# Kernel tuning notes

Measured on AMD Instinct MI355X. Metric: run time of the kernel, lower is better.

## Reference

```python
import jax, jax.numpy as jnp
import numpy as np
import math

B, T, E = 2, 2048, 1024
H = 16
D = E // H  # head_dim = 64

def setup_inputs() -> dict:
    key = jax.random.key(0)
    k1, k2, k3, k4, k5 = jax.random.split(key, 5)
    s = 0.02
    return {
        "x": jax.random.normal(k1, (B, T, E), dtype=jnp.float32),
        "W_attn": jax.random.normal(k2, (E, 3 * E), dtype=jnp.float32) * s,
        "b_attn": jax.random.normal(k3, (3 * E,), dtype=jnp.float32) * s,
        "W_proj": jax.random.normal(k4, (E, E), dtype=jnp.float32) * s,
        "b_proj": jax.random.normal(k5, (E,), dtype=jnp.float32) * s,
    }

def reference(x, W_attn, b_attn, W_proj, b_proj):
    Bx, Tx, Ex = x.shape
    qkv = x @ W_attn + b_attn                      # [B,T,3E]
    q, k, v = jnp.split(qkv, 3, axis=2)
    # [B,T,E] -> [B,H,T,D]
    def heads(t):
        return t.reshape(Bx, Tx, H, D).transpose(0, 2, 1, 3)
    q, k, v = heads(q), heads(k), heads(v)
    scores = jnp.einsum('bhqd,bhkd->bhqk', q, k) / math.sqrt(D)
    causal = jnp.tril(jnp.ones((Tx, Tx), dtype=bool))
    scores = jnp.where(causal, scores, -jnp.inf)
    attn = jax.nn.softmax(scores, axis=-1)
    out = jnp.einsum('bhqk,bhkd->bhqd', attn, v)   # [B,H,T,D]
    out = out.transpose(0, 2, 1, 3).reshape(Bx, Tx, Ex)
    return out @ W_proj + b_proj
```

## Files before the change

kernel.cpp:

```cpp
#include <hip/hip_runtime.h>


typedef unsigned short u16;
typedef unsigned int u32;
typedef __bf16 bf8 __attribute__((ext_vector_type(8)));
typedef float f32x4 __attribute__((ext_vector_type(4)));
typedef float f32x16 __attribute__((ext_vector_type(16)));
typedef u32 u32x4v __attribute__((ext_vector_type(4)));

__device__ __forceinline__ u16 f2b(float f) {
    return __builtin_bit_cast(u16, (__bf16)f);
}

__device__ __forceinline__ u32 pk2(float lo, float hi) {
    return (u32)f2b(lo) | ((u32)f2b(hi) << 16);
}

__device__ __forceinline__ f32x4 mfma16(bf8 a, bf8 b, f32x4 c) {
    return __builtin_amdgcn_mfma_f32_16x16x32_bf16(a, b, c, 0, 0, 0);
}

__device__ __forceinline__ f32x16 mfma32(bf8 a, bf8 b, f32x16 c) {
    return __builtin_amdgcn_mfma_f32_32x32x16_bf16(a, b, c, 0, 0, 0);
}

__device__ __forceinline__ float fexp2(float x) {
    return __builtin_amdgcn_exp2f(x);
}

__device__ __forceinline__ void gload_lds16(const u16* g, u16* l) {
    __builtin_amdgcn_global_load_lds(
        (__attribute__((address_space(1))) void*)(g),
        (__attribute__((address_space(3))) void*)(l), 16, 0, 0);
}

__global__ __launch_bounds__(256) void k_prep(const float* __restrict__ x,
                                              const float* __restrict__ Wa,
                                              const float* __restrict__ Wp,
                                              u16* __restrict__ Xb,
                                              u16* __restrict__ WtA,
                                              u16* __restrict__ WtP) {
    __shared__ float tile[64][65];
    int id = blockIdx.x, t = threadIdx.x;
    if (id < 4096) {
        int i = id * 256 + t;
        float4 v = ((const float4*)x)[i];
        ushort4 o;
        o.x = f2b(v.x); o.y = f2b(v.y); o.z = f2b(v.z); o.w = f2b(v.w);
        ((ushort4*)Xb)[i] = o;
        return;
    }
    const float* in; u16* out; int N, j;
    if (id < 4864) { j = id - 4096; in = Wa; out = WtA; N = 3072; }
    else           { j = id - 4864; in = Wp; out = WtP; N = 1024; }
    int k0 = (j & 15) * 64, n0 = (j >> 4) * 64;
    int c = t & 63, r0 = t >> 6;
#pragma unroll
    for (int i = 0; i < 16; ++i) {
        int r = r0 + i * 4;
        tile[r][c] = in[(size_t)(k0 + r) * N + n0 + c];
    }
    __syncthreads();
#pragma unroll
    for (int i = 0; i < 16; ++i) {
        int r = r0 + i * 4;
        out[(size_t)(n0 + r) * 1024 + k0 + c] = f2b(tile[c][r]);
    }
}

#define GEMM_STAGE(GA0, GA1, GB0, GB1, K, B)                                   \
    do {                                                                       \
        gload_lds16(GA0 + (K), As[B] + tid * 8);                               \
        gload_lds16(GA1 + (K), As[B] + (256 + tid) * 8);                       \
        gload_lds16(GB0 + (K), Bs[B] + tid * 8);                               \
        gload_lds16(GB1 + (K), Bs[B] + (256 + tid) * 8);                       \
    } while (0)

#define GEMM_CORE(Aptr, Bptr)                                                  \
    int tid = threadIdx.x;                                                     \
    int w = tid >> 6, lane = tid & 63, l16 = lane & 15, quad = lane >> 4;      \
    int m0 = blockIdx.x * 128, n0 = blockIdx.y * 128;                          \
    int wr = (w >> 1) * 64, wc = (w & 1) * 64;                                 \
    __shared__ u16 As[2][128 * 32];                                            \
    __shared__ u16 Bs[2][128 * 32];                                            \
    f32x4 acc[4][4];                                                           \
    _Pragma("unroll") for (int mi = 0; mi < 4; ++mi)                           \
        _Pragma("unroll") for (int ni = 0; ni < 4; ++ni)                       \
            _Pragma("unroll") for (int r = 0; r < 4; ++r) acc[mi][ni][r] = 0.f;\
    int srow0 = tid >> 2, srow1 = 64 + srow0;                                  \
    int slc = ((tid & 3) ^ ((tid >> 3) & 3)) * 8;      \
    const u16* gA0 = Aptr + (size_t)(m0 + srow0) * 1024 + slc;                 \
    const u16* gA1 = Aptr + (size_t)(m0 + srow1) * 1024 + slc;                 \
    const u16* gB0 = Bptr + (size_t)(n0 + srow0) * 1024 + slc;                 \
    const u16* gB1 = Bptr + (size_t)(n0 + srow1) * 1024 + slc;                 \
    int cq = (quad ^ ((l16 >> 1) & 3)) * 8;               \
    GEMM_STAGE(gA0, gA1, gB0, gB1, 0, 0);                                      \
    for (int it = 0; it < 32; ++it) {                                          \
        int pb = it & 1;                                                       \
        __syncthreads();                           \
        bf8 af[4], bf[4];                                                      \
        _Pragma("unroll") for (int mi = 0; mi < 4; ++mi)                       \
            af[mi] = *(const bf8*)(As[pb] + (wr + mi * 16 + l16) * 32 + cq);   \
        _Pragma("unroll") for (int ni = 0; ni < 4; ++ni)                       \
            bf[ni] = *(const bf8*)(Bs[pb] + (wc + ni * 16 + l16) * 32 + cq);   \
        if (it < 31) GEMM_STAGE(gA0, gA1, gB0, gB1, (it + 1) * 32, pb ^ 1);    \
        _Pragma("unroll") for (int mi = 0; mi < 4; ++mi)                       \
            _Pragma("unroll") for (int ni = 0; ni < 4; ++ni)                   \
                acc[mi][ni] = mfma16(af[mi], bf[ni], acc[mi][ni]);             \
    }

__global__ __launch_bounds__(256, 3) void k_qkv(const u16* __restrict__ Xb,
                                                const u16* __restrict__ WtA,
                                                const float* __restrict__ ba,
                                                u16* __restrict__ Qb,
                                                u16* __restrict__ Kb,
                                                u16* __restrict__ Vtb) {
    GEMM_CORE(Xb, WtA)
    int sel = n0 >> 10;
    u16* dst = sel == 0 ? Qb : (sel == 1 ? Kb : Vtb);
    const float qs = 0.18033688011112042f;
#pragma unroll
    for (int ni = 0; ni < 4; ++ni) {
        int n = n0 + wc + ni * 16 + l16;
        float bias = ba[n];
        int h = (n & 1023) >> 6;
        int d = n & 63;
#pragma unroll
        for (int mi = 0; mi < 4; ++mi)
#pragma unroll
            for (int r = 0; r < 4; ++r) {
                int m = m0 + wr + mi * 16 + quad * 4 + r;
                int bb = m >> 11, tt = m & 2047;
                float v = acc[mi][ni][r] + bias;
                size_t hb = (size_t)(bb * 16 + h);
                if (sel == 2)
                    dst[hb * 131072 + (size_t)(tt >> 6) * 4096 + d * 64 + (tt & 63)] = f2b(v);
                else
                    dst[(hb * 2048 + tt) * 64 + d] =
                        f2b(sel == 0 ? v * qs : v);
            }
    }
}

__global__ __launch_bounds__(256, 3) void k_proj(const u16* __restrict__ AO,
                                                 const u16* __restrict__ WtP,
                                                 const float* __restrict__ bp,
                                                 float* __restrict__ out) {
    GEMM_CORE(AO, WtP)
#pragma unroll
    for (int ni = 0; ni < 4; ++ni) {
        int n = n0 + wc + ni * 16 + l16;
        float bias = bp[n];
#pragma unroll
        for (int mi = 0; mi < 4; ++mi)
#pragma unroll
            for (int r = 0; r < 4; ++r) {
                int m = m0 + wr + mi * 16 + quad * 4 + r;
                out[(size_t)m * 1024 + n] = acc[mi][ni][r] + bias;
            }
    }
}


#define STAGE(KT, B) do {                                                     \
    int ci0_ = tid, ci1_ = 256 + tid;                                         \
    const u16* kt_ = Kh + (size_t)(KT) * 4096;                                \
    gload_lds16(kt_ + (ci0_ >> 3) * 64 +                                      \
                (((ci0_ & 7) ^ ((ci0_ >> 5) & 7)) * 8), KV[B][0] + ci0_ * 8); \
    gload_lds16(kt_ + (ci1_ >> 3) * 64 +                                      \
                (((ci1_ & 7) ^ ((ci1_ >> 5) & 7)) * 8), KV[B][0] + ci1_ * 8); \
    const u16* vt_ = Vh + (size_t)(KT) * 4096;                                \
    gload_lds16(vt_ + (ci0_ >> 3) * 64 +                                      \
                (((ci0_ & 7) ^ ((ci0_ >> 3) & 7)) * 8), KV[B][1] + ci0_ * 8); \
    gload_lds16(vt_ + (ci1_ >> 3) * 64 +                                      \
                (((ci1_ & 7) ^ ((ci1_ >> 3) & 7)) * 8), KV[B][1] + ci1_ * 8); \
} while (0)

#define PVSTEP(SG, BFR) do {                                                  \
    bf8 va_ = *(const bf8*)(vb_ + l31 * 64 +                                  \
                            (((2 * (SG) + h) ^ vswz) * 8));                   \
    bf8 vc_ = *(const bf8*)(vb_ + (32 + l31) * 64 +                           \
                            (((2 * (SG) + h) ^ vswz) * 8));                   \
    bf8 pf_ = __builtin_bit_cast(bf8, BFR);                                   \
    oT0 = mfma32(va_, pf_, oT0);                                              \
    oT1 = mfma32(vc_, pf_, oT1);                                              \
} while (0)

#define BFRAGS(PK, PP, B0, B1) do {                                           \
    B0[0] = h ? PP[2] : PK[0]; B0[1] = h ? PP[3] : PK[1];                     \
    B0[2] = h ? PK[2] : PP[0]; B0[3] = h ? PK[3] : PP[1];                     \
    B1[0] = h ? PP[6] : PK[4]; B1[1] = h ? PP[7] : PK[5];                     \
    B1[2] = h ? PK[6] : PP[4]; B1[3] = h ? PK[7] : PP[5];                     \
} while (0)

__global__ __launch_bounds__(256, 2) void k_attn(const u16* __restrict__ Qb,
                                                 const u16* __restrict__ Kb,
                                                 const u16* __restrict__ Vtb,
                                                 u16* __restrict__ AO) {
    int id = blockIdx.x;
    int bh = (id & 7) * 4 + ((id >> 3) & 3);
    int t  = 15 - (id >> 5);
    int tid = threadIdx.x;
    int w = tid >> 6, lane = tid & 63, l31 = lane & 31, h = lane >> 5;

    const u16* Qh = Qb  + (size_t)bh * 131072;
    const u16* Kh = Kb  + (size_t)bh * 131072;
    const u16* Vh = Vtb + (size_t)bh * 131072;

    __shared__ u16 KV[2][2][4096];

    int tq = t + 16 * w;
    int qr = tq * 32;
    int ktmax = tq >> 1;
    int nkt = ((t + 48) >> 1) + 1;

    bf8 qf[4];
#pragma unroll
    for (int s = 0; s < 4; ++s)
        qf[s] = *(const bf8*)(Qh + (size_t)(qr + l31) * 64 + s * 16 + h * 8);

    float l_acc = 0.f;
    f32x16 oT0, oT1;
#pragma unroll
    for (int r = 0; r < 16; ++r) { oT0[r] = 0.f; oT1[r] = 0.f; }

    int kswz = (l31 >> 2) & 7;
    int vswz = l31 & 7;

    STAGE(0, 0);
    for (int kt = 0; kt < nkt; ++kt) {
        int pb = kt & 1;
        __syncthreads();
        if (kt + 1 < nkt) STAGE(kt + 1, pb ^ 1);

        if (kt <= ktmax) {
            const u16* kb_ = KV[pb][0];
            const u16* vb_ = KV[pb][1];
            bool diag = (kt == ktmax);
            bool doK1 = !(diag && ((tq & 1) == 0));

            f32x16 sT0, sT1;
#pragma unroll
            for (int r = 0; r < 16; ++r) { sT0[r] = 0.f; sT1[r] = 0.f; }
#pragma unroll
            for (int s = 0; s < 4; ++s) {
                bf8 kf = *(const bf8*)(kb_ + l31 * 64 +
                                       (((2 * s + h) ^ kswz) * 8));
                sT0 = mfma32(kf, qf[s], sT0);
            }
            if (doK1) {
#pragma unroll
                for (int s = 0; s < 4; ++s) {
                    bf8 kf = *(const bf8*)(kb_ + (32 + l31) * 64 +
                                           (((2 * s + h) ^ kswz) * 8));
                    sT1 = mfma32(kf, qf[s], sT1);
                }
            }

            int kb0 = kt * 64, qg = qr + l31;
            if (diag) {
#pragma unroll
                for (int r = 0; r < 16; ++r) {
                    int krow = kb0 + (r & 3) + 8 * (r >> 2) + 4 * h;
                    sT0[r] = fexp2(krow <= qg ? sT0[r] : -1e30f);
                    l_acc += sT0[r];
                }
                if (doK1) {
#pragma unroll
                    for (int r = 0; r < 16; ++r) {
                        int krow = kb0 + 32 + (r & 3) + 8 * (r >> 2) + 4 * h;
                        sT1[r] = fexp2(krow <= qg ? sT1[r] : -1e30f);
                        l_acc += sT1[r];
                    }
                }
            } else {
#pragma unroll
                for (int r = 0; r < 16; ++r) {
                    sT0[r] = fexp2(sT0[r]); l_acc += sT0[r];
                }
#pragma unroll
                for (int r = 0; r < 16; ++r) {
                    sT1[r] = fexp2(sT1[r]); l_acc += sT1[r];
                }
            }

            u32 pka[8], ppa[8];
#pragma unroll
            for (int j = 0; j < 8; ++j)
                pka[j] = pk2(sT0[2 * j], sT0[2 * j + 1]);
#pragma unroll
            for (int j = 0; j < 8; ++j)
                ppa[j] = __shfl_xor(pka[j], 32, 64);
            u32x4v bf0, bf1;
            BFRAGS(pka, ppa, bf0, bf1);
            PVSTEP(0, bf0);
            PVSTEP(1, bf1);
            if (doK1) {
                u32 pkb[8], ppb[8];
#pragma unroll
                for (int j = 0; j < 8; ++j)
                    pkb[j] = pk2(sT1[2 * j], sT1[2 * j + 1]);
#pragma unroll
                for (int j = 0; j < 8; ++j)
                    ppb[j] = __shfl_xor(pkb[j], 32, 64);
                u32x4v bg0, bg1;
                BFRAGS(pkb, ppb, bg0, bg1);
                PVSTEP(2, bg0);
                PVSTEP(3, bg1);
            }
        }
    }

    __syncthreads();
    float lsum = l_acc + __shfl_xor(l_acc, 32, 64);
    float linv = __builtin_amdgcn_rcpf(lsum);

    u32* Ot = (u32*)(&KV[0][0][0]) + w * 1152;
#pragma unroll
    for (int j = 0; j < 8; ++j) {
        int col = 4 * (j >> 1) + 2 * h + (j & 1);
        Ot[l31 * 36 + col]      = pk2(oT0[2 * j] * linv, oT0[2 * j + 1] * linv);
        Ot[l31 * 36 + 16 + col] = pk2(oT1[2 * j] * linv, oT1[2 * j + 1] * linv);
    }
    asm volatile("s_waitcnt lgkmcnt(0)" ::: "memory");
    __builtin_amdgcn_sched_barrier(0);

    int q2 = lane >> 1, half = lane & 1;
    int eb = bh >> 4, eh = bh & 15;
    size_t row = (size_t)eb * 2048 + qr + q2;
    const u32* src = Ot + q2 * 36 + half * 16;
    u32* dstg = (u32*)(AO + row * 1024 + eh * 64) + half * 16;
#pragma unroll
    for (int c = 0; c < 4; ++c)
        *(u32x4v*)(dstg + 4 * c) = *(const u32x4v*)(src + 4 * c);
}

extern "C" void kernel_launch(void* const* d_in, const int* in_sizes, int n_in,
                              void* d_out, int out_size, void* d_ws, size_t ws_size,
                              hipStream_t stream) {
    const float* x  = (const float*)d_in[0];
    const float* Wa = (const float*)d_in[1];
    const float* ba = (const float*)d_in[2];
    const float* Wp = (const float*)d_in[3];
    const float* bp = (const float*)d_in[4];
    float* out = (float*)d_out;

    char* ws = (char*)d_ws;
    const size_t MB = 1024 * 1024;
    u16* Xb  = (u16*)(ws);
    u16* WtA = (u16*)(ws + 8  * MB);
    u16* WtP = (u16*)(ws + 14 * MB);
    u16* Qb  = (u16*)(ws + 16 * MB);
    u16* Kb  = (u16*)(ws + 24 * MB);
    u16* Vtb = (u16*)(ws + 32 * MB);
    u16* AO  = Xb;

    k_prep<<<dim3(5120),    dim3(256), 0, stream>>>(x, Wa, Wp, Xb, WtA, WtP);
    k_qkv <<<dim3(32, 24),  dim3(256), 0, stream>>>(Xb, WtA, ba, Qb, Kb, Vtb);
    k_attn<<<dim3(512),     dim3(256), 0, stream>>>(Qb, Kb, Vtb, AO);
    k_proj<<<dim3(32, 8),   dim3(256), 0, stream>>>(AO, WtP, bp, out);
}
```

Baseline: 182.1 us.

## Stage 128-key K/V blocks per barrier and use permlane32 swap for P repack

The attention loop now stages two 64-key K/V tiles per double-buffered stage, which halves the number of __syncthreads barriers and makes each prefetch larger. LDS use doubles to 64KB per block, which may limit occupancy at two blocks per CU. The P-fragment repack replaces eight cross-half shuffles plus selects with four v_permlane32_swap instructions. The K swizzle is unified with the V swizzle, which changes the LDS bank-conflict pattern. If nkt is odd, the last stage loads a tile past what was needed.

```diff
diff --git a/kernel.cpp b/kernel.cpp
--- a/kernel.cpp
+++ b/kernel.cpp
@@ -26,6 +26,10 @@
 
 __device__ __forceinline__ float fexp2(float x) {
     return __builtin_amdgcn_exp2f(x);
+}
+
+__device__ __forceinline__ void pl32swap(u32& a, u32& b) {
+    asm("v_permlane32_swap_b32 %0, %1" : "+v"(a), "+v"(b));
 }
 
 __device__ __forceinline__ void gload_lds16(const u16* g, u16* l) {
@@ -162,35 +166,40 @@
 }
 
 
-#define STAGE(KT, B) do {                                                     \
-    int ci0_ = tid, ci1_ = 256 + tid;                                         \
-    const u16* kt_ = Kh + (size_t)(KT) * 4096;                                \
-    gload_lds16(kt_ + (ci0_ >> 3) * 64 +                                      \
-                (((ci0_ & 7) ^ ((ci0_ >> 5) & 7)) * 8), KV[B][0] + ci0_ * 8); \
-    gload_lds16(kt_ + (ci1_ >> 3) * 64 +                                      \
-                (((ci1_ & 7) ^ ((ci1_ >> 5) & 7)) * 8), KV[B][0] + ci1_ * 8); \
-    const u16* vt_ = Vh + (size_t)(KT) * 4096;                                \
-    gload_lds16(vt_ + (ci0_ >> 3) * 64 +                                      \
-                (((ci0_ & 7) ^ ((ci0_ >> 3) & 7)) * 8), KV[B][1] + ci0_ * 8); \
-    gload_lds16(vt_ + (ci1_ >> 3) * 64 +                                      \
-                (((ci1_ & 7) ^ ((ci1_ >> 3) & 7)) * 8), KV[B][1] + ci1_ * 8); \
+#define STAGE128(KT2, B) do {                                                 \
+    const u16* kt_ = Kh + (size_t)(KT2) * 8192;                               \
+    _Pragma("unroll") for (int i_ = 0; i_ < 4; ++i_) {                        \
+        int ci_ = i_ * 256 + tid;             \
+        gload_lds16(kt_ + (ci_ >> 3) * 64 +                                   \
+                    (((ci_ & 7) ^ ((ci_ >> 3) & 7)) * 8), Ks[B] + ci_ * 8);   \
+    }                                                                         \
+    const u16* vt_ = Vh + (size_t)(KT2) * 8192;                               \
+    _Pragma("unroll") for (int i_ = 0; i_ < 4; ++i_) {                        \
+        int ci_ = i_ * 256 + tid;                  \
+        gload_lds16(vt_ + (ci_ >> 3) * 64 +                                   \
+                    (((ci_ & 7) ^ ((ci_ >> 3) & 7)) * 8), Vs[B] + ci_ * 8);   \
+    }                                                                         \
 } while (0)
 
 #define PVSTEP(SG, BFR) do {                                                  \
-    bf8 va_ = *(const bf8*)(vb_ + l31 * 64 +                                  \
-                            (((2 * (SG) + h) ^ vswz) * 8));                   \
+    bf8 va_ = *(const bf8*)(vb_ + l31 * 64 + (((2 * (SG) + h) ^ swz) * 8));   \
     bf8 vc_ = *(const bf8*)(vb_ + (32 + l31) * 64 +                           \
-                            (((2 * (SG) + h) ^ vswz) * 8));                   \
+                            (((2 * (SG) + h) ^ swz) * 8));                    \
     bf8 pf_ = __builtin_bit_cast(bf8, BFR);                                   \
     oT0 = mfma32(va_, pf_, oT0);                                              \
     oT1 = mfma32(vc_, pf_, oT1);                                              \
 } while (0)
 
-#define BFRAGS(PK, PP, B0, B1) do {                                           \
-    B0[0] = h ? PP[2] : PK[0]; B0[1] = h ? PP[3] : PK[1];                     \
-    B0[2] = h ? PK[2] : PP[0]; B0[3] = h ? PK[3] : PP[1];                     \
-    B1[0] = h ? PP[6] : PK[4]; B1[1] = h ? PP[7] : PK[5];                     \
-    B1[2] = h ? PK[6] : PP[4]; B1[3] = h ? PK[7] : PP[5];                     \
+#define REPACK_PV(ST, SG0, SG1) do {                                          \
+    u32 pk_[8];                                                               \
+    _Pragma("unroll") for (int j = 0; j < 8; ++j)                             \
+        pk_[j] = pk2(ST[2 * j], ST[2 * j + 1]);                               \
+    pl32swap(pk_[0], pk_[2]); pl32swap(pk_[1], pk_[3]);                       \
+    pl32swap(pk_[4], pk_[6]); pl32swap(pk_[5], pk_[7]);                       \
+    u32x4v f0_ = {pk_[0], pk_[1], pk_[2], pk_[3]};                            \
+    u32x4v f1_ = {pk_[4], pk_[5], pk_[6], pk_[7]};                            \
+    PVSTEP(SG0, f0_);                                                         \
+    PVSTEP(SG1, f1_);                                                         \
 } while (0)
 
 __global__ __launch_bounds__(256, 2) void k_attn(const u16* __restrict__ Qb,
@@ -207,12 +216,14 @@
     const u16* Kh = Kb  + (size_t)bh * 131072;
     const u16* Vh = Vtb + (size_t)bh * 131072;
 
-    __shared__ u16 KV[2][2][4096];
+    __shared__ u16 Ks[2][8192];
+    __shared__ u16 Vs[2][8192];
 
     int tq = t + 16 * w;
     int qr = tq * 32;
     int ktmax = tq >> 1;
     int nkt = ((t + 48) >> 1) + 1;
+    int nk2 = (nkt + 1) >> 1;
 
     bf8 qf[4];
 #pragma unroll
@@ -224,18 +235,20 @@
 #pragma unroll
     for (int r = 0; r < 16; ++r) { oT0[r] = 0.f; oT1[r] = 0.f; }
 
-    int kswz = (l31 >> 2) & 7;
-    int vswz = l31 & 7;
-
-    STAGE(0, 0);
-    for (int kt = 0; kt < nkt; ++kt) {
-        int pb = kt & 1;
+    int swz = l31 & 7;
+
+    STAGE128(0, 0);
+    for (int k2 = 0; k2 < nk2; ++k2) {
+        int pb = k2 & 1;
         __syncthreads();
-        if (kt + 1 < nkt) STAGE(kt + 1, pb ^ 1);
-
-        if (kt <= ktmax) {
-            const u16* kb_ = KV[pb][0];
-            const u16* vb_ = KV[pb][1];
+        if (k2 + 1 < nk2) STAGE128(k2 + 1, pb ^ 1);
+
+#pragma unroll
+        for (int s = 0; s < 2; ++s) {
+            int kt = 2 * k2 + s;
+            if (kt > ktmax) continue;
+            const u16* kb_ = Ks[pb] + s * 4096;
+            const u16* vb_ = Vs[pb] + s * 4096;
             bool diag = (kt == ktmax);
             bool doK1 = !(diag && ((tq & 1) == 0));
 
@@ -243,17 +256,17 @@
 #pragma unroll
             for (int r = 0; r < 16; ++r) { sT0[r] = 0.f; sT1[r] = 0.f; }
 #pragma unroll
-            for (int s = 0; s < 4; ++s) {
+            for (int d = 0; d < 4; ++d) {
                 bf8 kf = *(const bf8*)(kb_ + l31 * 64 +
-                                       (((2 * s + h) ^ kswz) * 8));
-                sT0 = mfma32(kf, qf[s], sT0);
+                                       (((2 * d + h) ^ swz) * 8));
+                sT0 = mfma32(kf, qf[d], sT0);
             }
             if (doK1) {
 #pragma unroll
-                for (int s = 0; s < 4; ++s) {
+                for (int d = 0; d < 4; ++d) {
                     bf8 kf = *(const bf8*)(kb_ + (32 + l31) * 64 +
-                                           (((2 * s + h) ^ kswz) * 8));
-                    sT1 = mfma32(kf, qf[s], sT1);
+                                           (((2 * d + h) ^ swz) * 8));
+                    sT1 = mfma32(kf, qf[d], sT1);
                 }
             }
 
@@ -284,30 +297,8 @@
                 }
             }
 
-            u32 pka[8], ppa[8];
-#pragma unroll
-            for (int j = 0; j < 8; ++j)
-                pka[j] = pk2(sT0[2 * j], sT0[2 * j + 1]);
-#pragma unroll
-            for (int j = 0; j < 8; ++j)
-                ppa[j] = __shfl_xor(pka[j], 32, 64);
-            u32x4v bf0, bf1;
-            BFRAGS(pka, ppa, bf0, bf1);
-            PVSTEP(0, bf0);
-            PVSTEP(1, bf1);
-            if (doK1) {
-                u32 pkb[8], ppb[8];
-#pragma unroll
-                for (int j = 0; j < 8; ++j)
-                    pkb[j] = pk2(sT1[2 * j], sT1[2 * j + 1]);
-#pragma unroll
-                for (int j = 0; j < 8; ++j)
-                    ppb[j] = __shfl_xor(pkb[j], 32, 64);
-                u32x4v bg0, bg1;
-                BFRAGS(pkb, ppb, bg0, bg1);
-                PVSTEP(2, bg0);
-                PVSTEP(3, bg1);
-            }
+            REPACK_PV(sT0, 0, 1);
+            if (doK1) REPACK_PV(sT1, 2, 3);
         }
     }
 
@@ -315,7 +306,7 @@
     float lsum = l_acc + __shfl_xor(l_acc, 32, 64);
     float linv = __builtin_amdgcn_rcpf(lsum);
 
-    u32* Ot = (u32*)(&KV[0][0][0]) + w * 1152;
+    u32* Ot = (u32*)(&Ks[0][0]) + w * 1152;
 #pragma unroll
     for (int j = 0; j < 8; ++j) {
         int col = 4 * (j >> 1) + 2 * h + (j & 1);
```

Result: faster. 177.4 us (-2.6%).
